# Performance work log

Hardware: AMD Instinct MI355X
Metric: run time of the kernel (lower is better)

The kernel has to match this reference:

```python
import jax, jax.numpy as jnp
import numpy as np

P = 16          # patch size (square)
HEADS = 8
DH = 64         # dim per head
SCALE = DH ** -0.5
EPS = 1e-5


def layernorm(x, g, b):
    mu = x.mean(-1, keepdims=True)
    var = ((x - mu) ** 2).mean(-1, keepdims=True)
    return (x - mu) * jax.lax.rsqrt(var + EPS) * g + b


def sattn(q, k, v):
    # q:[..., i, d], k/v:[..., j, d]; q already scaled
    sim = jnp.einsum('...id,...jd->...ij', q, k)
    a = jax.nn.softmax(sim, axis=-1)
    return jnp.einsum('...ij,...jd->...id', a, v)


def split_heads(t, b, N):
    return t.reshape(b, N, HEADS, DH).transpose(0, 2, 1, 3).reshape(b * HEADS, N, DH)


def merge_heads(t, b, N):
    return t.reshape(b, HEADS, N, DH).transpose(0, 2, 1, 3).reshape(b, N, HEADS * DH)


def qkv_cls(x, ln_g, ln_b, qkv_w):
    b, N, _ = x.shape
    xn = layernorm(x, ln_g, ln_b)
    q, k, v = jnp.split(xn @ qkv_w, 3, axis=-1)
    q = split_heads(q, b, N) * SCALE
    k = split_heads(k, b, N)
    v = split_heads(v, b, N)
    cls_out = sattn(q[:, :1], k, v)          # cls attends to everything
    return q[:, 1:], k[:, 1:], v[:, 1:], k[:, :1], v[:, :1], cls_out


def time_attention(x, ln_g, ln_b, qkv_w, out_w, out_b, f, n):
    b, N, _ = x.shape
    q_, k_, v_, cls_k, cls_v, cls_out = qkv_cls(x, ln_g, ln_b, qkv_w)
    bh = b * HEADS
    resh = lambda t: t.reshape(bh, f, n, DH).transpose(0, 2, 1, 3)  # 'b (f n) d -> (b n) f d' kept as [bh,n,f,d]
    q_, k_, v_ = resh(q_), resh(k_), resh(v_)
    ck = jnp.broadcast_to(cls_k[:, None], (bh, n, 1, DH))
    cv = jnp.broadcast_to(cls_v[:, None], (bh, n, 1, DH))
    out = sattn(q_, jnp.concatenate([ck, k_], 2), jnp.concatenate([cv, v_], 2))
    out = out.transpose(0, 2, 1, 3).reshape(bh, f * n, DH)
    out = jnp.concatenate([cls_out, out], axis=1)
    return merge_heads(out, b, N) @ out_w + out_b


def space_attention(x, ln_g, ln_b, qkv_w, out_w, out_b, f, n):
    b, N, _ = x.shape
    q_, k_, v_, cls_k, cls_v, cls_out = qkv_cls(x, ln_g, ln_b, qkv_w)
    bh = b * HEADS
    resh = lambda t: t.reshape(bh, f, n, DH)  # 'b (f n) d -> (b f) n d' kept as [bh,f,n,d]
    q_, k_, v_ = resh(q_), resh(k_), resh(v_)
    m = n // 2
    ck = jnp.broadcast_to(cls_k[:, None], (bh, f, 1, DH))
    cv = jnp.broadcast_to(cls_v[:, None], (bh, f, 1, DH))
    # mutual attention: first half queries attend to [cls, second half], and vice versa
    out1 = sattn(q_[:, :, :m], jnp.concatenate([ck, k_[:, :, m:]], 2), jnp.concatenate([cv, v_[:, :, m:]], 2))
    out2 = sattn(q_[:, :, m:], jnp.concatenate([ck, k_[:, :, :m]], 2), jnp.concatenate([cv, v_[:, :, :m]], 2))
    out = jnp.concatenate([out1, out2], axis=2).reshape(bh, f * n, DH)
    out = jnp.concatenate([cls_out, out], axis=1)
    return merge_heads(out, b, N) @ out_w + out_b


def geglu_ff(x, ln_g, ln_b, w1, b1, w2, b2):
    xn = layernorm(x, ln_g, ln_b)
    h = xn @ w1 + b1
    u, g = jnp.split(h, 2, axis=-1)
    return (u * jax.nn.gelu(g, approximate=False)) @ w2 + b2


def setup_inputs() -> dict:
    key = jax.random.key(0)
    ks = jax.random.split(key, 12)
    D, DEPTH, NC = 512, 12, 60
    inner = HEADS * DH
    B, F, C, H, W = 1, 4, 3, 480, 640
    n = (H // P) * (W // P)        # 1200
    N = F * n + 1                  # 4801
    pd = C * P * P                 # 768
    s = 0.02
    rn = lambda k, sh: jax.random.normal(k, sh, jnp.float32) * s
    z = lambda sh: jnp.zeros(sh, jnp.float32)
    o = lambda sh: jnp.ones(sh, jnp.float32)
    return {
        'video': jax.random.normal(ks[0], (B, F, C, H, W), jnp.float32),
        'patch_w': rn(ks[1], (pd, D)), 'patch_b': z((D,)),
        'pos_emb': rn(ks[2], (N, D)),
        'cls_token': rn(ks[3], (1, D)),
        't_ln_g': o((DEPTH, D)), 't_ln_b': z((DEPTH, D)),
        't_qkv_w': rn(ks[4], (DEPTH, D, 3 * inner)),
        't_out_w': rn(ks[5], (DEPTH, inner, D)), 't_out_b': z((DEPTH, D)),
        's_ln_g': o((DEPTH, D)), 's_ln_b': z((DEPTH, D)),
        's_qkv_w': rn(ks[6], (DEPTH, D, 3 * inner)),
        's_out_w': rn(ks[7], (DEPTH, inner, D)), 's_out_b': z((DEPTH, D)),
        'f_ln_g': o((DEPTH, D)), 'f_ln_b': z((DEPTH, D)),
        'f_w1': rn(ks[8], (DEPTH, D, 8 * D)), 'f_b1': z((DEPTH, 8 * D)),
        'f_w2': rn(ks[9], (DEPTH, 4 * D, D)), 'f_b2': z((DEPTH, D)),
        'o_ln_g': o((D,)), 'o_ln_b': z((D,)),
        'o_w': rn(ks[10], (D, NC)), 'o_b': z((NC,)),
    }


def reference(video, patch_w, patch_b, pos_emb, cls_token,
              t_ln_g, t_ln_b, t_qkv_w, t_out_w, t_out_b,
              s_ln_g, s_ln_b, s_qkv_w, s_out_w, s_out_b,
              f_ln_g, f_ln_b, f_w1, f_b1, f_w2, f_b2,
              o_ln_g, o_ln_b, o_w, o_b):
    b, f, c, H, W = video.shape
    hh, ww = H // P, W // P
    n = hh * ww
    wh = ww // 2
    half = W // 2

    def patchify(v):  # v: [b,f,c,H,W/2] -> [b, f*hh*wh, P*P*c]
        v = v.reshape(b, f, c, hh, P, wh, P)
        v = v.transpose(0, 1, 3, 5, 4, 6, 2)  # b f h w p1 p2 c
        return v.reshape(b, f * hh * wh, P * P * c)

    tok = jnp.concatenate([patchify(video[..., :half]), patchify(video[..., half:])], axis=1)
    tok = tok @ patch_w + patch_b
    x = jnp.concatenate([jnp.broadcast_to(cls_token[None], (b, 1, tok.shape[-1])), tok], axis=1)
    x = x + pos_emb[: x.shape[1]]

    depth = t_qkv_w.shape[0]
    for i in range(depth):
        x = time_attention(x, t_ln_g[i], t_ln_b[i], t_qkv_w[i], t_out_w[i], t_out_b[i], f, n) + x
        x = space_attention(x, s_ln_g[i], s_ln_b[i], s_qkv_w[i], s_out_w[i], s_out_b[i], f, n) + x
        x = geglu_ff(x, f_ln_g[i], f_ln_b[i], f_w1[i], f_b1[i], f_w2[i], f_b2[i]) + x

    cls = layernorm(x[:, 0], o_ln_g, o_ln_b)
    return cls @ o_w + o_b
```

## Files before the change

kernel.cpp:

```cpp
#include <hip/hip_runtime.h>
#include <cmath>


#define NT      4801
#define NP      4800
#define MP      4864
#define DM      512
#define QKV_ST  1536
#define LN_EPS  1e-5f
#define NCH     49

typedef __attribute__((ext_vector_type(8))) short bf16x8;
typedef __attribute__((ext_vector_type(4))) float f32x4;

__device__ __forceinline__ unsigned short f2b(float f) {
    union { float f; unsigned int u; } x; x.f = f;
    unsigned int r = (x.u + 0x7FFFu + ((x.u >> 16) & 1u)) >> 16;
    return (unsigned short)r;
}
__device__ __forceinline__ float b2f(unsigned short b) {
    union { unsigned int u; float f; } x; x.u = ((unsigned int)b) << 16;
    return x.f;
}
__device__ __forceinline__ unsigned int pack2(float a, float b) {
    return (unsigned int)f2b(a) | ((unsigned int)f2b(b) << 16);
}

__device__ __forceinline__ void gl_lds16(const void* g, void* l) {
    __builtin_amdgcn_global_load_lds(
        (__attribute__((address_space(1))) unsigned int*)(unsigned long long)(uintptr_t)g,
        (__attribute__((address_space(3))) unsigned int*)l, 16, 0, 0);
}

__global__ void patchify_kernel(const float* __restrict__ video, unsigned short* __restrict__ out)
{
    int idx = blockIdx.x * 256 + threadIdx.x;
    if (idx >= NP * 768) return;
    int tok = idx / 768, e = idx % 768;
    int c  = e % 3;
    int pe = e / 3;
    int p2 = pe % 16, p1 = pe / 16;
    int half = tok / 2400, r = tok % 2400;
    int f = r / 600, rr = r % 600;
    int hi = rr / 20, wi = rr % 20;
    int row = hi * 16 + p1;
    int col = half * 320 + wi * 16 + p2;
    out[idx] = f2b(video[(((size_t)f * 3 + c) * 480 + row) * 640 + col]);
}

__global__ void cls_init_kernel(const float* __restrict__ cls_token,
                                const float* __restrict__ pos, float* __restrict__ X)
{
    int d = blockIdx.x * 256 + threadIdx.x;
    if (d < DM) X[d] = cls_token[d] + pos[d];
}

__device__ __forceinline__ void transpose_tile(const float* __restrict__ in,
                                               unsigned short* __restrict__ out,
                                               int K, int N, int tile)
{
    __shared__ float T[32][33];
    int ntk = K / 32;
    int kt = tile % ntk, nt = tile / ntk;
    int k0 = kt * 32, n0 = nt * 32;
    int tx = threadIdx.x & 31, ty = threadIdx.x >> 5;
    #pragma unroll
    for (int i = 0; i < 4; i++)
        T[ty + 8 * i][tx] = in[(size_t)(k0 + ty + 8 * i) * N + n0 + tx];
    __syncthreads();
    #pragma unroll
    for (int i = 0; i < 4; i++)
        out[(size_t)(n0 + ty + 8 * i) * K + k0 + tx] = f2b(T[tx][ty + 8 * i]);
}

__global__ __launch_bounds__(256) void convertT_layer(
    const float* __restrict__ w0, const float* __restrict__ w1,
    const float* __restrict__ w2, const float* __restrict__ w3,
    const float* __restrict__ w4, const float* __restrict__ w5,
    unsigned short* __restrict__ out)
{
    int t = blockIdx.x;
    if      (t <  768) transpose_tile(w0, out + 0,       512, 1536, t);
    else if (t < 1024) transpose_tile(w1, out + 786432,  512,  512, t - 768);
    else if (t < 1792) transpose_tile(w2, out + 1048576, 512, 1536, t - 1024);
    else if (t < 2048) transpose_tile(w3, out + 1835008, 512,  512, t - 1792);
    else if (t < 4096) transpose_tile(w4, out + 2097152, 512, 4096, t - 2048);
    else               transpose_tile(w5, out + 4194304, 2048, 512, t - 4096);
}

__global__ __launch_bounds__(256) void convertT_one(
    const float* __restrict__ in, unsigned short* __restrict__ out, int K, int N)
{
    transpose_tile(in, out, K, N, blockIdx.x);
}

template<bool OB16>
__global__ __launch_bounds__(256, 2) void mfma_gemm(
    const unsigned short* __restrict__ A, const unsigned short* __restrict__ BT,
    const float* __restrict__ bias, const float* __restrict__ add,
    void* __restrict__ C, int Mv, int N, int K)
{
    __shared__ short Asm[128 * 64];
    __shared__ short Bsm[128 * 64];
    const int tid = threadIdx.x, w = tid >> 6, lane = tid & 63;
    const int row0 = blockIdx.y * 128, col0 = blockIdx.x * 128;
    const int wm = w >> 1, wn = w & 1;
    const int l15 = lane & 15, quad = lane >> 4;

    f32x4 acc[4][4] = {};

    int arows[4], aqs[4];
    #pragma unroll
    for (int i = 0; i < 4; i++) {
        int s = (w * 4 + i) * 64 + lane;
        arows[i] = s >> 3;
        aqs[i]   = (s & 7) ^ ((s >> 3) & 7);
    }

    for (int k0 = 0; k0 < K; k0 += 64) {
        __syncthreads();
        #pragma unroll
        for (int i = 0; i < 4; i++) {
            gl_lds16(A  + (size_t)(row0 + arows[i]) * K + k0 + aqs[i] * 8,
                     &Asm[(w * 4 + i) * 512]);
            gl_lds16(BT + (size_t)(col0 + arows[i]) * K + k0 + aqs[i] * 8,
                     &Bsm[(w * 4 + i) * 512]);
        }
        __syncthreads();
        #pragma unroll
        for (int ks = 0; ks < 2; ks++) {
            bf16x8 af[4], bfr[4];
            #pragma unroll
            for (int i = 0; i < 4; i++) {
                int m  = wm * 64 + i * 16 + l15;
                int pa = (ks * 4 + quad) ^ (m & 7);
                af[i]  = *(const bf16x8*)&Asm[m * 64 + pa * 8];
                int n  = wn * 64 + i * 16 + l15;
                int pb = (ks * 4 + quad) ^ (n & 7);
                bfr[i] = *(const bf16x8*)&Bsm[n * 64 + pb * 8];
            }
            #pragma unroll
            for (int i = 0; i < 4; i++)
                #pragma unroll
                for (int j = 0; j < 4; j++)
                    acc[i][j] = __builtin_amdgcn_mfma_f32_16x16x32_bf16(
                                    af[i], bfr[j], acc[i][j], 0, 0, 0);
        }
    }

    #pragma unroll
    for (int i = 0; i < 4; i++) {
        #pragma unroll
        for (int r = 0; r < 4; r++) {
            int row = row0 + wm * 64 + i * 16 + quad * 4 + r;
            if (row >= Mv) continue;
            #pragma unroll
            for (int j = 0; j < 4; j++) {
                int col = col0 + wn * 64 + j * 16 + l15;
                float v = acc[i][j][r];
                if (bias) v += bias[col];
                if (add)  v += add[(size_t)row * N + col];
                if (OB16) ((unsigned short*)C)[(size_t)row * N + col] = f2b(v);
                else      ((float*)C)[(size_t)row * N + col] = v;
            }
        }
    }
}

__global__ __launch_bounds__(256) void ln_bf16(
    const float* __restrict__ x, const float* __restrict__ g,
    const float* __restrict__ b, unsigned short* __restrict__ y, int M)
{
    int wid = threadIdx.x >> 6, lane = threadIdx.x & 63;
    int row = blockIdx.x * 4 + wid;
    if (row >= M) return;
    const float4* xr = (const float4*)(x + (size_t)row * DM);
    float4 v0 = xr[lane * 2], v1 = xr[lane * 2 + 1];
    float s  = v0.x + v0.y + v0.z + v0.w + v1.x + v1.y + v1.z + v1.w;
    float s2 = v0.x*v0.x + v0.y*v0.y + v0.z*v0.z + v0.w*v0.w
             + v1.x*v1.x + v1.y*v1.y + v1.z*v1.z + v1.w*v1.w;
    #pragma unroll
    for (int off = 32; off >= 1; off >>= 1) {
        s  += __shfl_xor(s, off);
        s2 += __shfl_xor(s2, off);
    }
    float mu = s * (1.f / DM);
    float var = s2 * (1.f / DM) - mu * mu;
    float r = rsqrtf(var + LN_EPS);
    const float4* gv = (const float4*)g;
    const float4* bv = (const float4*)b;
    unsigned int* yr = (unsigned int*)(y + (size_t)row * DM);
    #pragma unroll
    for (int i = 0; i < 2; i++) {
        float4 v = (i == 0) ? v0 : v1;
        float4 gg = gv[lane * 2 + i], bb = bv[lane * 2 + i];
        float ox = (v.x - mu) * r * gg.x + bb.x;
        float oy = (v.y - mu) * r * gg.y + bb.y;
        float oz = (v.z - mu) * r * gg.z + bb.z;
        float ow = (v.w - mu) * r * gg.w + bb.w;
        yr[lane * 4 + i * 2 + 0] = pack2(ox, oy);
        yr[lane * 4 + i * 2 + 1] = pack2(oz, ow);
    }
}

__global__ __launch_bounds__(256, 2) void time_attn(
    const unsigned short* __restrict__ qkv, unsigned short* __restrict__ out)
{
    int t = blockIdx.x * 256 + threadIdx.x;
    if (t >= 8 * NP) return;
    int h = t / NP, j = t - h * NP;
    int pos = j % 1200;
    union { bf16x8 v; unsigned short u[8]; } ld;
    float q[64];
    const unsigned short* qp = qkv + (size_t)(j + 1) * QKV_ST + h * 64;
    #pragma unroll
    for (int c = 0; c < 8; c++) {
        ld.v = *(const bf16x8*)(qp + c * 8);
        #pragma unroll
        for (int e = 0; e < 8; e++) q[c * 8 + e] = b2f(ld.u[e]) * 0.125f;
    }
    int rows[5] = {0, pos + 1, pos + 1201, pos + 2401, pos + 3601};
    float s[5];
    #pragma unroll
    for (int kk = 0; kk < 5; kk++) {
        const unsigned short* kp = qkv + (size_t)rows[kk] * QKV_ST + 512 + h * 64;
        float ss = 0.f;
        #pragma unroll
        for (int c = 0; c < 8; c++) {
            ld.v = *(const bf16x8*)(kp + c * 8);
            #pragma unroll
            for (int e = 0; e < 8; e++) ss += q[c * 8 + e] * b2f(ld.u[e]);
        }
        s[kk] = ss;
    }
    float mx = s[0];
    #pragma unroll
    for (int kk = 1; kk < 5; kk++) mx = fmaxf(mx, s[kk]);
    float e5[5], l = 0.f;
    #pragma unroll
    for (int kk = 0; kk < 5; kk++) { e5[kk] = __expf(s[kk] - mx); l += e5[kk]; }
    float rl = 1.f / l;
    float acc[64];
    #pragma unroll
    for (int d = 0; d < 64; d++) acc[d] = 0.f;
    #pragma unroll
    for (int kk = 0; kk < 5; kk++) {
        float p = e5[kk] * rl;
        const unsigned short* vp = qkv + (size_t)rows[kk] * QKV_ST + 1024 + h * 64;
        #pragma unroll
        for (int c = 0; c < 8; c++) {
            ld.v = *(const bf16x8*)(vp + c * 8);
            #pragma unroll
            for (int e = 0; e < 8; e++) acc[c * 8 + e] += p * b2f(ld.u[e]);
        }
    }
    unsigned int* op = (unsigned int*)(out + (size_t)(j + 1) * DM + h * 64);
    #pragma unroll
    for (int d2 = 0; d2 < 32; d2++) op[d2] = pack2(acc[2 * d2], acc[2 * d2 + 1]);
}

#define SPAD 72
__global__ __launch_bounds__(256, 2) void space_attn_mfma(
    const unsigned short* __restrict__ qkv, unsigned short* __restrict__ out)
{
    __shared__ short Ksm[64 * SPAD];
    __shared__ short VTsm[64 * SPAD];
    __shared__ short Psm[4][32 * SPAD];
    int qt = blockIdx.x, h = blockIdx.y, g = blockIdx.z;
    int f = g >> 1, half = g & 1;
    int tid = threadIdx.x, w = tid >> 6, lane = tid & 63;
    int l15 = lane & 15, quad = lane >> 4;

    int qrow_base = qt * 128 + w * 32;
    int qb = 1 + f * 1200 + half * 600;
    int kb = 1 + f * 1200 + (1 - half) * 600;

    bf16x8 aQ[2][2];
    #pragma unroll
    for (int mf = 0; mf < 2; mf++) {
        int qr = qrow_base + mf * 16 + l15;
        int qtok = qb + ((qr < 600) ? qr : 0);
        const unsigned short* qp = qkv + (size_t)qtok * QKV_ST + h * 64;
        #pragma unroll
        for (int ks = 0; ks < 2; ks++)
            aQ[mf][ks] = *(const bf16x8*)(qp + ks * 32 + quad * 8);
    }

    f32x4 O[2][4] = {};
    float mrow[2][4], lrow[2][4];
    #pragma unroll
    for (int mf = 0; mf < 2; mf++)
        #pragma unroll
        for (int r = 0; r < 4; r++) { mrow[mf][r] = -1e30f; lrow[mf][r] = 0.f; }

    for (int kt = 0; kt < 10; kt++) {
        __syncthreads();
        #pragma unroll
        for (int it = 0; it < 2; it++) {
            int c = tid + it * 256;
            int row = c >> 3, dc = (c & 7) * 8;
            int kidx = kt * 64 + row;
            int tok = (kidx == 0) ? 0 : ((kidx <= 600) ? kb + kidx - 1 : 0);
            const unsigned short* kp = qkv + (size_t)tok * QKV_ST + 512 + h * 64 + dc;
            *(bf16x8*)&Ksm[row * SPAD + dc] = *(const bf16x8*)kp;
            union { bf16x8 v; unsigned short u[8]; } vv;
            vv.v = *(const bf16x8*)(kp + 512);
            #pragma unroll
            for (int e = 0; e < 8; e++)
                VTsm[(dc + e) * SPAD + row] = vv.u[e];
        }
        __syncthreads();

        f32x4 S[2][4] = {};
        #pragma unroll
        for (int ks = 0; ks < 2; ks++) {
            bf16x8 bK[4];
            #pragma unroll
            for (int nf = 0; nf < 4; nf++)
                bK[nf] = *(const bf16x8*)&Ksm[(nf * 16 + l15) * SPAD + ks * 32 + quad * 8];
            #pragma unroll
            for (int mf = 0; mf < 2; mf++)
                #pragma unroll
                for (int nf = 0; nf < 4; nf++)
                    S[mf][nf] = __builtin_amdgcn_mfma_f32_16x16x32_bf16(
                                    aQ[mf][ks], bK[nf], S[mf][nf], 0, 0, 0);
        }

        #pragma unroll
        for (int mf = 0; mf < 2; mf++) {
            float pv[4][4];
            float lm[4] = {-1e30f, -1e30f, -1e30f, -1e30f};
            #pragma unroll
            for (int nf = 0; nf < 4; nf++) {
                int kidx = kt * 64 + nf * 16 + l15;
                bool valid = kidx <= 600;
                #pragma unroll
                for (int r = 0; r < 4; r++) {
                    float s = valid ? S[mf][nf][r] * 0.125f : -1e30f;
                    pv[nf][r] = s;
                    lm[r] = fmaxf(lm[r], s);
                }
            }
            #pragma unroll
            for (int off = 1; off < 16; off <<= 1)
                #pragma unroll
                for (int r = 0; r < 4; r++)
                    lm[r] = fmaxf(lm[r], __shfl_xor(lm[r], off));
            #pragma unroll
            for (int r = 0; r < 4; r++) {
                float nm = fmaxf(mrow[mf][r], lm[r]);
                float c = __expf(mrow[mf][r] - nm);
                mrow[mf][r] = nm;
                lrow[mf][r] *= c;
                #pragma unroll
                for (int nf = 0; nf < 4; nf++) O[mf][nf][r] *= c;
            }
            float rs[4] = {0.f, 0.f, 0.f, 0.f};
            #pragma unroll
            for (int nf = 0; nf < 4; nf++)
                #pragma unroll
                for (int r = 0; r < 4; r++) {
                    float p = __expf(pv[nf][r] - mrow[mf][r]);
                    pv[nf][r] = p;
                    rs[r] += p;
                }
            #pragma unroll
            for (int off = 1; off < 16; off <<= 1)
                #pragma unroll
                for (int r = 0; r < 4; r++)
                    rs[r] += __shfl_xor(rs[r], off);
            #pragma unroll
            for (int r = 0; r < 4; r++) lrow[mf][r] += rs[r];
            #pragma unroll
            for (int nf = 0; nf < 4; nf++)
                #pragma unroll
                for (int r = 0; r < 4; r++)
                    Psm[w][(mf * 16 + quad * 4 + r) * SPAD + nf * 16 + l15] = (short)f2b(pv[nf][r]);
        }
        asm volatile("s_waitcnt lgkmcnt(0)" ::: "memory");

        #pragma unroll
        for (int ks2 = 0; ks2 < 2; ks2++) {
            bf16x8 aP[2], bV[4];
            #pragma unroll
            for (int mf = 0; mf < 2; mf++)
                aP[mf] = *(const bf16x8*)&Psm[w][(mf * 16 + l15) * SPAD + ks2 * 32 + quad * 8];
            #pragma unroll
            for (int nf = 0; nf < 4; nf++)
                bV[nf] = *(const bf16x8*)&VTsm[(nf * 16 + l15) * SPAD + ks2 * 32 + quad * 8];
            #pragma unroll
            for (int mf = 0; mf < 2; mf++)
                #pragma unroll
                for (int nf = 0; nf < 4; nf++)
                    O[mf][nf] = __builtin_amdgcn_mfma_f32_16x16x32_bf16(
                                    aP[mf], bV[nf], O[mf][nf], 0, 0, 0);
        }
    }

    #pragma unroll
    for (int mf = 0; mf < 2; mf++)
        #pragma unroll
        for (int r = 0; r < 4; r++) {
            int qr = qrow_base + mf * 16 + quad * 4 + r;
            if (qr >= 600) continue;
            int qtok = qb + qr;
            float rl = 1.f / lrow[mf][r];
            #pragma unroll
            for (int nf = 0; nf < 4; nf++)
                out[(size_t)qtok * DM + h * 64 + nf * 16 + l15] = f2b(O[mf][nf][r] * rl);
        }
}

__global__ __launch_bounds__(256) void cls_attn_part(
    const unsigned short* __restrict__ qkv, float* __restrict__ part)
{
    int ch = blockIdx.x, h = blockIdx.y;
    int wid = threadIdx.x >> 6, lane = threadIdx.x & 63;
    __shared__ float sm[4], sl[4], sa[4][64];
    float qv = b2f(qkv[h * 64 + lane]) * 0.125f;
    int k0 = ch * 100 + wid * 25;
    float m = -1e30f, l = 0.f, acc = 0.f;
    for (int i = 0; i < 25; i += 2) {
        int key0 = k0 + i, key1 = key0 + 1;
        bool ok0 = key0 < NT;
        bool ok1 = (i + 1 < 25) && (key1 < NT);
        const unsigned short* kr0 = qkv + (size_t)(ok0 ? key0 : 0) * QKV_ST + 512 + h * 64;
        const unsigned short* kr1 = qkv + (size_t)(ok1 ? key1 : 0) * QKV_ST + 512 + h * 64;
        float s0 = qv * b2f(kr0[lane]);
        float v0 = b2f(kr0[512 + lane]);
        float s1 = qv * b2f(kr1[lane]);
        float v1 = b2f(kr1[512 + lane]);
        #pragma unroll
        for (int off = 32; off >= 1; off >>= 1) {
            s0 += __shfl_xor(s0, off);
            s1 += __shfl_xor(s1, off);
        }
        float nm = m;
        if (ok0) nm = fmaxf(nm, s0);
        if (ok1) nm = fmaxf(nm, s1);
        float c  = __expf(m - nm);
        float p0 = ok0 ? __expf(s0 - nm) : 0.f;
        float p1 = ok1 ? __expf(s1 - nm) : 0.f;
        l   = l * c + p0 + p1;
        acc = acc * c + p0 * v0 + p1 * v1;
        m = nm;
    }
    if (lane == 0) { sm[wid] = m; sl[wid] = l; }
    sa[wid][lane] = acc;
    __syncthreads();
    if (wid == 0) {
        float M2 = fmaxf(fmaxf(sm[0], sm[1]), fmaxf(sm[2], sm[3]));
        float L = 0.f, o = 0.f;
        #pragma unroll
        for (int w = 0; w < 4; w++) {
            float c = __expf(sm[w] - M2);
            L += sl[w] * c;
            o += sa[w][lane] * c;
        }
        float* p = part + ((size_t)h * NCH + ch) * 68;
        if (lane == 0) { p[0] = M2; p[1] = L; }
        p[4 + lane] = o;
    }
}

__global__ __launch_bounds__(64) void cls_attn_reduce(
    const float* __restrict__ part, unsigned short* __restrict__ out)
{
    int h = blockIdx.x, lane = threadIdx.x;
    float m = -1e30f, l = 0.f, acc = 0.f;
    for (int c = 0; c < NCH; c++) {
        const float* p = part + ((size_t)h * NCH + c) * 68;
        float cm = p[0], cl = p[1], ca = p[4 + lane];
        float nm = fmaxf(m, cm);
        float e1 = __expf(m - nm), e2 = __expf(cm - nm);
        l   = l * e1 + cl * e2;
        acc = acc * e1 + ca * e2;
        m = nm;
    }
    out[h * 64 + lane] = f2b(acc / l);
}

__global__ __launch_bounds__(256) void geglu_kernel(
    const unsigned short* __restrict__ h, unsigned short* __restrict__ out)
{
    int idx = blockIdx.x * 256 + threadIdx.x;
    if (idx >= NT * 256) return;
    int r = idx >> 8, cc = (idx & 255) * 8;
    const unsigned short* up = h + (size_t)r * 4096 + cc;
    const unsigned short* gp = up + 2048;
    float o[8];
    #pragma unroll
    for (int e = 0; e < 8; e++) {
        float u = b2f(up[e]), gg = b2f(gp[e]);
        o[e] = u * 0.5f * gg * (1.f + erff(gg * 0.70710678f));
    }
    unsigned int* op = (unsigned int*)(out + (size_t)r * 2048 + cc);
    #pragma unroll
    for (int e = 0; e < 4; e++) op[e] = pack2(o[2 * e], o[2 * e + 1]);
}

__global__ __launch_bounds__(64) void head_kernel(
    const float* __restrict__ x, const float* __restrict__ g,
    const float* __restrict__ b, const float* __restrict__ w,
    const float* __restrict__ ob, float* __restrict__ out)
{
    __shared__ float xn[DM];
    int lane = threadIdx.x;
    const float4* xr = (const float4*)x;
    float4 v0 = xr[lane * 2], v1 = xr[lane * 2 + 1];
    float s  = v0.x + v0.y + v0.z + v0.w + v1.x + v1.y + v1.z + v1.w;
    float s2 = v0.x*v0.x + v0.y*v0.y + v0.z*v0.z + v0.w*v0.w
             + v1.x*v1.x + v1.y*v1.y + v1.z*v1.z + v1.w*v1.w;
    #pragma unroll
    for (int off = 32; off >= 1; off >>= 1) {
        s  += __shfl_xor(s, off);
        s2 += __shfl_xor(s2, off);
    }
    float mu = s * (1.f / DM);
    float var = s2 * (1.f / DM) - mu * mu;
    float r = rsqrtf(var + LN_EPS);
    #pragma unroll
    for (int i = 0; i < 8; i++) {
        int d = lane * 8 + i;
        xn[d] = (x[d] - mu) * r * g[d] + b[d];
    }
    __syncthreads();
    if (lane < 60) {
        float a = ob[lane];
        for (int d = 0; d < DM; d++) a += xn[d] * w[d * 60 + lane];
        out[lane] = a;
    }
}

extern "C" void kernel_launch(void* const* d_in, const int* in_sizes, int n_in,
                              void* d_out, int out_size, void* d_ws, size_t ws_size,
                              hipStream_t stream)
{
    const float* video     = (const float*)d_in[0];
    const float* patch_w   = (const float*)d_in[1];
    const float* patch_b   = (const float*)d_in[2];
    const float* pos_emb   = (const float*)d_in[3];
    const float* cls_token = (const float*)d_in[4];
    const float* t_ln_g    = (const float*)d_in[5];
    const float* t_ln_b    = (const float*)d_in[6];
    const float* t_qkv_w   = (const float*)d_in[7];
    const float* t_out_w   = (const float*)d_in[8];
    const float* t_out_b   = (const float*)d_in[9];
    const float* s_ln_g    = (const float*)d_in[10];
    const float* s_ln_b    = (const float*)d_in[11];
    const float* s_qkv_w   = (const float*)d_in[12];
    const float* s_out_w   = (const float*)d_in[13];
    const float* s_out_b   = (const float*)d_in[14];
    const float* f_ln_g    = (const float*)d_in[15];
    const float* f_ln_b    = (const float*)d_in[16];
    const float* f_w1      = (const float*)d_in[17];
    const float* f_b1      = (const float*)d_in[18];
    const float* f_w2      = (const float*)d_in[19];
    const float* f_b2      = (const float*)d_in[20];
    const float* o_ln_g    = (const float*)d_in[21];
    const float* o_ln_b    = (const float*)d_in[22];
    const float* o_w       = (const float*)d_in[23];
    const float* o_b       = (const float*)d_in[24];

    char* ws = (char*)d_ws;
    size_t o = 0;
    float*          X    = (float*)(ws + o);          o += (size_t)(MP + 1) * 512 * 4;
    unsigned short* XN   = (unsigned short*)(ws + o); o += (size_t)MP * 512 * 2;
    unsigned short* QKV  = (unsigned short*)(ws + o); o += (size_t)MP * 1536 * 2;
    unsigned short* H16  = (unsigned short*)(ws + o); o += (size_t)MP * 4096 * 2;
    unsigned short* MID  = (unsigned short*)(ws + o); o += (size_t)MP * 2048 * 2;
    unsigned short* PT   = (unsigned short*)(ws + o); o += (size_t)MP * 768 * 2;
    unsigned short* W16  = (unsigned short*)(ws + o); o += (size_t)5242880 * 2;
    unsigned short* PW16 = (unsigned short*)(ws + o); o += (size_t)512 * 768 * 2;
    float*          CP   = (float*)(ws + o);          o += (size_t)8 * NCH * 68 * 4;

    patchify_kernel<<<(NP * 768 + 255) / 256, 256, 0, stream>>>(video, PT);
    cls_init_kernel<<<2, 256, 0, stream>>>(cls_token, pos_emb, X);
    convertT_one<<<(768 / 32) * (512 / 32), 256, 0, stream>>>(patch_w, PW16, 768, 512);
    mfma_gemm<false><<<dim3(4, 38), 256, 0, stream>>>(PT, PW16, patch_b, pos_emb + DM,
                                                      X + DM, NP, DM, 768);

    dim3 g_qkv(12, 38), g_out(4, 38), g_ff1(32, 38), g_ff2(4, 38);
    for (int i = 0; i < 12; i++) {
        convertT_layer<<<5120, 256, 0, stream>>>(
            t_qkv_w + (size_t)i * 512 * 1536, t_out_w + (size_t)i * 512 * 512,
            s_qkv_w + (size_t)i * 512 * 1536, s_out_w + (size_t)i * 512 * 512,
            f_w1 + (size_t)i * 512 * 4096, f_w2 + (size_t)i * 2048 * 512, W16);

        ln_bf16<<<1201, 256, 0, stream>>>(X, t_ln_g + i * DM, t_ln_b + i * DM, XN, NT);
        mfma_gemm<true><<<g_qkv, 256, 0, stream>>>(XN, W16 + 0, nullptr, nullptr,
                                                   QKV, NT, QKV_ST, DM);
        time_attn<<<150, 256, 0, stream>>>(QKV, MID);
        cls_attn_part<<<dim3(NCH, 8), 256, 0, stream>>>(QKV, CP);
        cls_attn_reduce<<<8, 64, 0, stream>>>(CP, MID);
        mfma_gemm<false><<<g_out, 256, 0, stream>>>(MID, W16 + 786432, t_out_b + i * DM,
                                                    X, X, NT, DM, DM);
        ln_bf16<<<1201, 256, 0, stream>>>(X, s_ln_g + i * DM, s_ln_b + i * DM, XN, NT);
        mfma_gemm<true><<<g_qkv, 256, 0, stream>>>(XN, W16 + 1048576, nullptr, nullptr,
                                                   QKV, NT, QKV_ST, DM);
        space_attn_mfma<<<dim3(5, 8, 8), 256, 0, stream>>>(QKV, MID);
        cls_attn_part<<<dim3(NCH, 8), 256, 0, stream>>>(QKV, CP);
        cls_attn_reduce<<<8, 64, 0, stream>>>(CP, MID);
        mfma_gemm<false><<<g_out, 256, 0, stream>>>(MID, W16 + 1835008, s_out_b + i * DM,
                                                    X, X, NT, DM, DM);
        ln_bf16<<<1201, 256, 0, stream>>>(X, f_ln_g + i * DM, f_ln_b + i * DM, XN, NT);
        mfma_gemm<true><<<g_ff1, 256, 0, stream>>>(XN, W16 + 2097152, f_b1 + i * 4096,
                                                   nullptr, H16, NT, 4096, DM);
        geglu_kernel<<<(NT * 256 + 255) / 256, 256, 0, stream>>>(H16, MID);
        mfma_gemm<false><<<g_ff2, 256, 0, stream>>>(MID, W16 + 4194304, f_b2 + i * DM,
                                                    X, X, NT, DM, 2048);
    }

    head_kernel<<<1, 64, 0, stream>>>(X, o_ln_g, o_ln_b, o_w, o_b, (float*)d_out);
}
```

Baseline: 4.640 ms.

## Split-K the N=512 output and FF2 GEMMs with atomic accumulation into the residual

Adds a split-K GEMM variant that divides the K dimension across grid z and accumulates partial tiles straight into the fp32 residual X with atomic adds. Only split 0 adds the bias. It replaces the out-projection GEMMs (2 splits) and FF2 (4 splits), whose 4x38 grids were too small to fill the GPU. The launch bound on the GEMMs also rises to 4 blocks per CU. The cost is extra atomic traffic on X, non-deterministic summation order, and possible register pressure from the higher occupancy target.

```diff
diff --git a/kernel.cpp b/kernel.cpp
--- a/kernel.cpp
+++ b/kernel.cpp
@@ -95,7 +95,7 @@
 }
 
 template<bool OB16>
-__global__ __launch_bounds__(256, 2) void mfma_gemm(
+__global__ __launch_bounds__(256, 4) void mfma_gemm(
     const unsigned short* __restrict__ A, const unsigned short* __restrict__ BT,
     const float* __restrict__ bias, const float* __restrict__ add,
     void* __restrict__ C, int Mv, int N, int K)
@@ -162,6 +162,79 @@
                 if (add)  v += add[(size_t)row * N + col];
                 if (OB16) ((unsigned short*)C)[(size_t)row * N + col] = f2b(v);
                 else      ((float*)C)[(size_t)row * N + col] = v;
+            }
+        }
+    }
+}
+
+template<int SPLITS>
+__global__ __launch_bounds__(256, 4) void mfma_gemm_sk(
+    const unsigned short* __restrict__ A, const unsigned short* __restrict__ BT,
+    const float* __restrict__ bias, float* __restrict__ C, int Mv, int N, int K)
+{
+    __shared__ short Asm[128 * 64];
+    __shared__ short Bsm[128 * 64];
+    const int tid = threadIdx.x, w = tid >> 6, lane = tid & 63;
+    const int row0 = blockIdx.y * 128, col0 = blockIdx.x * 128;
+    const int wm = w >> 1, wn = w & 1;
+    const int l15 = lane & 15, quad = lane >> 4;
+    const int kchunk = K / SPLITS;
+    const int kbeg = blockIdx.z * kchunk;
+
+    f32x4 acc[4][4] = {};
+
+    int arows[4], aqs[4];
+    #pragma unroll
+    for (int i = 0; i < 4; i++) {
+        int s = (w * 4 + i) * 64 + lane;
+        arows[i] = s >> 3;
+        aqs[i]   = (s & 7) ^ ((s >> 3) & 7);
+    }
+
+    for (int k0 = kbeg; k0 < kbeg + kchunk; k0 += 64) {
+        __syncthreads();
+        #pragma unroll
+        for (int i = 0; i < 4; i++) {
+            gl_lds16(A  + (size_t)(row0 + arows[i]) * K + k0 + aqs[i] * 8,
+                     &Asm[(w * 4 + i) * 512]);
+            gl_lds16(BT + (size_t)(col0 + arows[i]) * K + k0 + aqs[i] * 8,
+                     &Bsm[(w * 4 + i) * 512]);
+        }
+        __syncthreads();
+        #pragma unroll
+        for (int ks = 0; ks < 2; ks++) {
+            bf16x8 af[4], bfr[4];
+            #pragma unroll
+            for (int i = 0; i < 4; i++) {
+                int m  = wm * 64 + i * 16 + l15;
+                int pa = (ks * 4 + quad) ^ (m & 7);
+                af[i]  = *(const bf16x8*)&Asm[m * 64 + pa * 8];
+                int n  = wn * 64 + i * 16 + l15;
+                int pb = (ks * 4 + quad) ^ (n & 7);
+                bfr[i] = *(const bf16x8*)&Bsm[n * 64 + pb * 8];
+            }
+            #pragma unroll
+            for (int i = 0; i < 4; i++)
+                #pragma unroll
+                for (int j = 0; j < 4; j++)
+                    acc[i][j] = __builtin_amdgcn_mfma_f32_16x16x32_bf16(
+                                    af[i], bfr[j], acc[i][j], 0, 0, 0);
+        }
+    }
+
+    const bool addb = (blockIdx.z == 0) && (bias != nullptr);
+    #pragma unroll
+    for (int i = 0; i < 4; i++) {
+        #pragma unroll
+        for (int r = 0; r < 4; r++) {
+            int row = row0 + wm * 64 + i * 16 + quad * 4 + r;
+            if (row >= Mv) continue;
+            #pragma unroll
+            for (int j = 0; j < 4; j++) {
+                int col = col0 + wn * 64 + j * 16 + l15;
+                float v = acc[i][j][r];
+                if (addb) v += bias[col];
+                unsafeAtomicAdd(&C[(size_t)row * N + col], v);
             }
         }
     }
@@ -580,7 +653,8 @@
     mfma_gemm<false><<<dim3(4, 38), 256, 0, stream>>>(PT, PW16, patch_b, pos_emb + DM,
                                                       X + DM, NP, DM, 768);
 
-    dim3 g_qkv(12, 38), g_out(4, 38), g_ff1(32, 38), g_ff2(4, 38);
+    dim3 g_qkv(12, 38), g_ff1(32, 38);
+    dim3 g_out_sk(4, 38, 2), g_ff2_sk(4, 38, 4);
     for (int i = 0; i < 12; i++) {
         convertT_layer<<<5120, 256, 0, stream>>>(
             t_qkv_w + (size_t)i * 512 * 1536, t_out_w + (size_t)i * 512 * 512,
@@ -593,22 +667,22 @@
         time_attn<<<150, 256, 0, stream>>>(QKV, MID);
         cls_attn_part<<<dim3(NCH, 8), 256, 0, stream>>>(QKV, CP);
         cls_attn_reduce<<<8, 64, 0, stream>>>(CP, MID);
-        mfma_gemm<false><<<g_out, 256, 0, stream>>>(MID, W16 + 786432, t_out_b + i * DM,
-                                                    X, X, NT, DM, DM);
+        mfma_gemm_sk<2><<<g_out_sk, 256, 0, stream>>>(MID, W16 + 786432, t_out_b + i * DM,
+                                                      X, NT, DM, DM);
         ln_bf16<<<1201, 256, 0, stream>>>(X, s_ln_g + i * DM, s_ln_b + i * DM, XN, NT);
         mfma_gemm<true><<<g_qkv, 256, 0, stream>>>(XN, W16 + 1048576, nullptr, nullptr,
                                                    QKV, NT, QKV_ST, DM);
         space_attn_mfma<<<dim3(5, 8, 8), 256, 0, stream>>>(QKV, MID);
         cls_attn_part<<<dim3(NCH, 8), 256, 0, stream>>>(QKV, CP);
         cls_attn_reduce<<<8, 64, 0, stream>>>(CP, MID);
-        mfma_gemm<false><<<g_out, 256, 0, stream>>>(MID, W16 + 1835008, s_out_b + i * DM,
-                                                    X, X, NT, DM, DM);
+        mfma_gemm_sk<2><<<g_out_sk, 256, 0, stream>>>(MID, W16 + 1835008, s_out_b + i * DM,
+                                                      X, NT, DM, DM);
         ln_bf16<<<1201, 256, 0, stream>>>(X, f_ln_g + i * DM, f_ln_b + i * DM, XN, NT);
         mfma_gemm<true><<<g_ff1, 256, 0, stream>>>(XN, W16 + 2097152, f_b1 + i * 4096,
                                                    nullptr, H16, NT, 4096, DM);
         geglu_kernel<<<(NT * 256 + 255) / 256, 256, 0, stream>>>(H16, MID);
-        mfma_gemm<false><<<g_ff2, 256, 0, stream>>>(MID, W16 + 4194304, f_b2 + i * DM,
-                                                    X, X, NT, DM, 2048);
+        mfma_gemm_sk<4><<<g_ff2_sk, 256, 0, stream>>>(MID, W16 + 4194304, f_b2 + i * DM,
+                                                      X, NT, DM, 2048);
     }
 
     head_kernel<<<1, 64, 0, stream>>>(X, o_ln_g, o_ln_b, o_w, o_b, (float*)d_out);
```

New measurement: 4.474 ms. 3.6% less time.
